# Optimization experiments

Hardware: AMD Instinct MI355X
Metric: run time of the kernel (lower is better)

## Reference

```python
import jax, jax.numpy as jnp
from jax import lax
import numpy as np

# Geometry derived from module.calibrate() for input [2,64,768,768], k=3, s=1, bcount=(16,16)
N, CIN, COUT, H, W = 2, 64, 64, 768, 768
K, STRIDE = 3, 1
BC = 16            # block count per spatial dim
PAD = 1            # total pad 2 -> 1 each side (H and W)
BSIZE = 50         # gathered block size (input space, padded input is 770)
BOUT = 48          # conv output size per block
BSTR = 48          # block stride (= bsize - k + stride); also scatter stride
NBLK = 256
BN_EPS = 1e-3


def setup_inputs() -> dict:
    key = jax.random.key(0)
    ks = jax.random.split(key, 7)
    x = jax.random.normal(ks[0], (N, CIN, H, W), jnp.float32)
    conv_w = jax.random.normal(ks[1], (COUT, CIN, K, K), jnp.float32) * 0.05
    conv_b = jax.random.normal(ks[2], (COUT,), jnp.float32) * 0.1
    gamma = jax.random.uniform(ks[3], (COUT,), jnp.float32, 0.5, 1.5)
    beta = jax.random.normal(ks[4], (COUT,), jnp.float32) * 0.1
    run_mean = jax.random.normal(ks[5], (COUT,), jnp.float32) * 0.1
    run_var = jax.random.uniform(ks[6], (COUT,), jnp.float32, 0.5, 1.5)
    # unique active blocks (n, bh, bw) as in ReduceMask.active_block_indices
    rng = np.random.default_rng(0)
    all_blocks = np.stack(np.meshgrid(np.arange(N), np.arange(BC), np.arange(BC),
                                      indexing='ij'), axis=-1).reshape(-1, 3)
    sel = rng.permutation(all_blocks.shape[0])[:NBLK]
    abi = jnp.asarray(all_blocks[sel], jnp.int32)
    return dict(x=x, conv_w=conv_w, conv_b=conv_b, gamma=gamma, beta=beta,
                run_mean=run_mean, run_var=run_var, active_block_indices=abi)


def reference(x, conv_w, conv_b, gamma, beta, run_mean, run_var, active_block_indices):
    # pad as in F.pad(padding_params)
    xp = jnp.pad(x, ((0, 0), (0, 0), (PAD, PAD), (PAD, PAD)))  # [N,C,770,770]
    nidx = active_block_indices[:, 0]                          # [B]
    hh = active_block_indices[:, 1][:, None] * BSTR + jnp.arange(BSIZE)[None, :]  # [B,50]
    ww = active_block_indices[:, 2][:, None] * BSTR + jnp.arange(BSIZE)[None, :]  # [B,50]
    # sparse_gather: extract [B,50,50,C] blocks (vectorized advanced indexing)
    xp_nhwc = xp.transpose(0, 2, 3, 1)
    p = xp_nhwc[nidx[:, None, None], hh[:, :, None], ww[:, None, :]]   # [B,50,50,C]
    p = p.transpose(0, 3, 1, 2)                                        # [B,C,50,50]
    # conv2d (VALID) + bias
    q = lax.conv_general_dilated(p, conv_w, (STRIDE, STRIDE), 'VALID')
    q = q + conv_b[None, :, None, None]                                # [B,COUT,48,48]
    # BatchNorm (inference: running stats) + ReLU
    inv = gamma / jnp.sqrt(run_var + BN_EPS)
    q = q * inv[None, :, None, None] + (beta - run_mean * inv)[None, :, None, None]
    q = jax.nn.relu(q)
    # sparse_scatter (add=False) into [N,COUT,768,768]; blocks are non-overlapping
    ho = active_block_indices[:, 1][:, None] * BSTR + jnp.arange(BOUT)[None, :]
    wo = active_block_indices[:, 2][:, None] * BSTR + jnp.arange(BOUT)[None, :]
    y = jnp.zeros((N, H, W, COUT), x.dtype)
    y = y.at[nidx[:, None, None], ho[:, :, None], wo[:, None, :]].set(q.transpose(0, 2, 3, 1))
    return y.transpose(0, 3, 1, 2)
```

## Files before the change

kernel.cpp:

```cpp
#include <hip/hip_runtime.h>


typedef __attribute__((ext_vector_type(8))) short short8;
typedef __attribute__((ext_vector_type(4))) float floatx4;

#define WS_SCALE 0
#define WS_SHIFT 64
#define WS_FLAGS 128
#define WS_WA    640

#define CONV_WGS 1536
#define ZERO_WGS 4096

#define LDS_BUF 4864

__device__ __forceinline__ short f2bf(float f) {
  unsigned u = __builtin_bit_cast(unsigned, f);
  u += 0x7fffu + ((u >> 16) & 1u);
  return (short)(u >> 16);
}

__global__ __launch_bounds__(256) void prep_kernel(
    const float* __restrict__ conv_w,
    const float* __restrict__ conv_b,
    const float* __restrict__ gamma,
    const float* __restrict__ beta,
    const float* __restrict__ run_mean,
    const float* __restrict__ run_var,
    const int* __restrict__ abi,
    float* __restrict__ ws) {
  int tid = threadIdx.x;
  if (blockIdx.x == 0) {
    int* flags = (int*)(ws + WS_FLAGS);
    flags[tid] = 0;
    flags[tid + 256] = 0;
    __syncthreads();
    int n = abi[3 * tid + 0];
    int bh = abi[3 * tid + 1];
    int bw = abi[3 * tid + 2];
    flags[n * 256 + bh * 16 + bw] = 1;
    if (tid < 64) {
      float inv = gamma[tid] * rsqrtf(run_var[tid] + 1e-3f);
      ws[WS_SCALE + tid] = inv;
      ws[WS_SHIFT + tid] = (conv_b[tid] - run_mean[tid]) * inv + beta[tid];
    }
  }
  short* wa = (short*)(ws + WS_WA);
  for (int d = blockIdx.x * 256 + tid; d < 49152; d += 64 * 256) {
    int j = d & 7;
    int q = (d >> 3) & 3;
    int cout = (d >> 5) & 63;
    int ks = d >> 11;
    int kt = ks % 3;
    int cc = ks / 3;
    int tap = kt * 4 + q;
    short v = 0;
    if (tap < 9) {
      int ci = cc * 8 + j;
      int dy = tap / 3;
      int dx = tap - dy * 3;
      v = f2bf(conv_w[((cout * 64 + ci) * 3 + dy) * 3 + dx]);
    }
    wa[d] = v;
  }
}

__global__ __launch_bounds__(512, 4) void main_kernel(
    const float* __restrict__ x,
    const float* __restrict__ ws_f,
    const int* __restrict__ abi,
    float* __restrict__ out) {
  __shared__ __align__(16) short lds[3 * LDS_BUF];

  int b = blockIdx.x;
  int tid = threadIdx.x;

  if (b >= CONV_WGS) {
    const int* flags = (const int*)(ws_f + WS_FLAGS);
    int z = b - CONV_WGS;
    int tile = z >> 3;
    int part = z & 7;
    if (flags[tile]) return;
    int n = tile >> 8;
    int bh = (tile >> 4) & 15;
    int bw = tile & 15;
    float* base = out + (((n * 64 + part * 8) * 768 + bh * 48)) * 768 + bw * 48;
    float4 zv = make_float4(0.f, 0.f, 0.f, 0.f);
#pragma unroll
    for (int i = 0; i < 9; ++i) {
      int idx = i * 512 + tid;
      int f = idx % 12;
      int t2 = idx / 12;
      int rr = t2 % 48;
      int c = t2 / 48;
      *((float4*)(base + (c * 768 + rr) * (size_t)768) + f) = zv;
    }
    return;
  }

  int blk = b / 6;
  int strip = b - blk * 6;
  int n = abi[3 * blk + 0];
  int bh = abi[3 * blk + 1];
  int bw = abi[3 * blk + 2];
  int h0 = bh * 48 + strip * 8;
  int w0 = bw * 48;

  int lane = tid & 63;
  int wv = tid >> 6;
  int ln15 = lane & 15;
  int quad = lane >> 4;

  const float* xn = x + (size_t)n * 64 * 768 * 768;
  const short* wa = (const short*)(ws_f + WS_WA);
  const short* wap = wa + ln15 * 32 + quad * 8;

  if (tid < 8) {
#pragma unroll
    for (int bb = 0; bb < 3; ++bb) {
      lds[bb * LDS_BUF + 4560 + tid] = 0;
      lds[bb * LDS_BUF + 4704 + tid] = 0;
      lds[bb * LDS_BUF + 4848 + tid] = 0;
    }
  }

  int bA[3];
#pragma unroll
  for (int kt = 0; kt < 3; ++kt) {
    int tap = kt * 4 + quad;
    if (tap < 9) {
      int dy = tap / 3;
      int dx = tap - dy * 3;
      int cx = ln15 + dx;
      bA[kt] = ((wv + dy) * 57 + cx + (cx >> 3)) * 16;
    } else {
      bA[kt] = 9120;
    }
  }

  auto load_chunk = [&](int cc8, float4* pf) {
#pragma unroll
    for (int i = 0; i < 3; ++i) {
      int e = i * 512 + tid;
      float4 v = make_float4(0.f, 0.f, 0.f, 0.f);
      if (e < 1120) {
        int f = e % 14;
        int t = e / 14;
        int r = t % 10;
        int ci = t / 10;
        int gh = h0 - 1 + r;
        int gw0 = w0 - 4 + 4 * f;
        if ((unsigned)gh < 768u) {
          const float* rp = xn + ((size_t)(cc8 + ci) * 768 + gh) * 768;
          if (gw0 >= 0 && gw0 <= 764) {
            v = *(const float4*)(rp + gw0);
          } else {
#pragma unroll
            for (int j = 0; j < 4; ++j) {
              int gw = gw0 + j;
              if ((unsigned)gw < 768u) ((float*)&v)[j] = rp[gw];
            }
          }
        }
      }
      pf[i] = v;
    }
  };
  auto store_chunk = [&](short* dst, const float4* pf) {
#pragma unroll
    for (int i = 0; i < 3; ++i) {
      int e = i * 512 + tid;
      if (e < 1120) {
        int f = e % 14;
        int t = e / 14;
        int r = t % 10;
        int ci = t / 10;
        const float* vp = (const float*)&pf[i];
#pragma unroll
        for (int j = 0; j < 4; ++j) {
          int c = 4 * f - 3 + j;
          if ((unsigned)c < 50u) {
            int u = r * 57 + c + (c >> 3);
            dst[u * 8 + ci] = f2bf(vp[j]);
          }
        }
      }
    }
  };

  float4 pf[3];
  load_chunk(0, pf);
  store_chunk(lds, pf);
  load_chunk(8, pf);

  floatx4 acc[3][4];
#pragma unroll
  for (int c16 = 0; c16 < 3; ++c16)
#pragma unroll
    for (int mt = 0; mt < 4; ++mt)
      acc[c16][mt] = (floatx4){0.f, 0.f, 0.f, 0.f};

  int rb = 0;
  for (int cc = 0; cc < 8; ++cc) {
    __syncthreads();
    int sb = (rb == 2) ? 0 : rb + 1;
    if (cc < 7) store_chunk(lds + sb * LDS_BUF, pf);
    if (cc < 6) load_chunk((cc + 2) * 8, pf);
    const char* lb = (const char*)(lds + rb * LDS_BUF);
#pragma unroll
    for (int kt = 0; kt < 3; ++kt) {
      int ks = cc * 3 + kt;
      short8 af[4];
#pragma unroll
      for (int mt = 0; mt < 4; ++mt)
        af[mt] = *(const short8*)(wap + ks * 2048 + mt * 512);
#pragma unroll
      for (int c16 = 0; c16 < 3; ++c16) {
        short8 bf = *(const short8*)(lb + bA[kt] + c16 * 288);
#pragma unroll
        for (int mt = 0; mt < 4; ++mt)
          acc[c16][mt] = __builtin_amdgcn_mfma_f32_16x16x32_bf16(
              af[mt], bf, acc[c16][mt], 0, 0, 0);
      }
    }
    rb = sb;
  }

  const float* scale = ws_f + WS_SCALE;
  const float* shift = ws_f + WS_SHIFT;
  float* op = out + (size_t)n * 64 * 768 * 768 + (size_t)(h0 + wv) * 768 + (w0 + ln15);
#pragma unroll
  for (int mt = 0; mt < 4; ++mt) {
#pragma unroll
    for (int reg = 0; reg < 4; ++reg) {
      int cout = mt * 16 + quad * 4 + reg;
      float sc = scale[cout];
      float sh = shift[cout];
#pragma unroll
      for (int c16 = 0; c16 < 3; ++c16) {
        float vv = fmaf(acc[c16][mt][reg], sc, sh);
        vv = vv > 0.f ? vv : 0.f;
        op[(size_t)cout * 589824 + c16 * 16] = vv;
      }
    }
  }
}

extern "C" void kernel_launch(void* const* d_in, const int* in_sizes, int n_in,
                              void* d_out, int out_size, void* d_ws, size_t ws_size,
                              hipStream_t stream) {
  const float* x = (const float*)d_in[0];
  const float* conv_w = (const float*)d_in[1];
  const float* conv_b = (const float*)d_in[2];
  const float* gamma = (const float*)d_in[3];
  const float* beta = (const float*)d_in[4];
  const float* run_mean = (const float*)d_in[5];
  const float* run_var = (const float*)d_in[6];
  const int* abi = (const int*)d_in[7];
  float* out = (float*)d_out;
  float* ws = (float*)d_ws;

  prep_kernel<<<64, 256, 0, stream>>>(conv_w, conv_b, gamma, beta,
                                      run_mean, run_var, abi, ws);
  main_kernel<<<CONV_WGS + ZERO_WGS, 512, 0, stream>>>(x, ws, abi, out);
}
```

Measured before the change: 585.5 us.

## Stage conv weight slices into LDS via async global_load_lds double buffer

Weight fragments were read by every wave straight from global memory. They are now copied per channel-chunk into a double-buffered LDS slice using global_load_lds, and the prep kernel reorders the weights so each lane's fragment is contiguous. The input staging drops from a triple to a double buffer, with one barrier at the end of each iteration. The aim is to cut repeated global and L2 traffic for weights and hide it behind compute. Total LDS per workgroup grows to about 44KB, which may reduce how many workgroups fit per CU. The barrier may also force waits on in-flight prefetch loads.

Result: faster. 558.0 us (-4.7%).

```diff
diff --git a/kernel.cpp b/kernel.cpp
--- a/kernel.cpp
+++ b/kernel.cpp
@@ -13,6 +13,7 @@
 #define ZERO_WGS 4096
 
 #define LDS_BUF 4864
+#define WSLICE  6144
 
 __device__ __forceinline__ short f2bf(float f) {
   unsigned u = __builtin_bit_cast(unsigned, f);
@@ -48,14 +49,18 @@
   short* wa = (short*)(ws + WS_WA);
   for (int d = blockIdx.x * 256 + tid; d < 49152; d += 64 * 256) {
     int j = d & 7;
-    int q = (d >> 3) & 3;
-    int cout = (d >> 5) & 63;
-    int ks = d >> 11;
+    int g = d >> 3;
+    int i4q = g & 63;
+    int ln15 = i4q >> 2;
+    int quad = i4q & 3;
+    int mt = (g >> 6) & 3;
+    int ks = g >> 8;
     int kt = ks % 3;
     int cc = ks / 3;
-    int tap = kt * 4 + q;
+    int tap = kt * 4 + quad;
     short v = 0;
     if (tap < 9) {
+      int cout = mt * 16 + ln15;
       int ci = cc * 8 + j;
       int dy = tap / 3;
       int dx = tap - dy * 3;
@@ -70,7 +75,8 @@
     const float* __restrict__ ws_f,
     const int* __restrict__ abi,
     float* __restrict__ out) {
-  __shared__ __align__(16) short lds[3 * LDS_BUF];
+  __shared__ __align__(16) short lds_i[2][LDS_BUF];
+  __shared__ __align__(16) short lds_w[2][WSLICE];
 
   int b = blockIdx.x;
   int tid = threadIdx.x;
@@ -113,14 +119,14 @@
 
   const float* xn = x + (size_t)n * 64 * 768 * 768;
   const short* wa = (const short*)(ws_f + WS_WA);
-  const short* wap = wa + ln15 * 32 + quad * 8;
+  int wOff = (ln15 * 4 + quad) * 8;
 
   if (tid < 8) {
 #pragma unroll
-    for (int bb = 0; bb < 3; ++bb) {
-      lds[bb * LDS_BUF + 4560 + tid] = 0;
-      lds[bb * LDS_BUF + 4704 + tid] = 0;
-      lds[bb * LDS_BUF + 4848 + tid] = 0;
+    for (int bb = 0; bb < 2; ++bb) {
+      lds_i[bb][4560 + tid] = 0;
+      lds_i[bb][4704 + tid] = 0;
+      lds_i[bb][4848 + tid] = 0;
     }
   }
 
@@ -137,6 +143,18 @@
       bA[kt] = 9120;
     }
   }
+
+  auto wload = [&](int cc, int wsel) {
+    const short* src = wa + (size_t)cc * WSLICE;
+    __builtin_amdgcn_global_load_lds(
+        (const __attribute__((address_space(1))) void*)(src + tid * 8),
+        (__attribute__((address_space(3))) void*)&lds_w[wsel][tid * 8], 16, 0, 0);
+    if (tid < 256)
+      __builtin_amdgcn_global_load_lds(
+          (const __attribute__((address_space(1))) void*)(src + 4096 + tid * 8),
+          (__attribute__((address_space(3))) void*)&lds_w[wsel][4096 + tid * 8],
+          16, 0, 0);
+  };
 
   auto load_chunk = [&](int cc8, float4* pf) {
 #pragma unroll
@@ -189,8 +207,9 @@
   };
 
   float4 pf[3];
+  wload(0, 0);
   load_chunk(0, pf);
-  store_chunk(lds, pf);
+  store_chunk(lds_i[0], pf);
   load_chunk(8, pf);
 
   floatx4 acc[3][4];
@@ -200,20 +219,23 @@
     for (int mt = 0; mt < 4; ++mt)
       acc[c16][mt] = (floatx4){0.f, 0.f, 0.f, 0.f};
 
-  int rb = 0;
+  __syncthreads();
+
   for (int cc = 0; cc < 8; ++cc) {
-    __syncthreads();
-    int sb = (rb == 2) ? 0 : rb + 1;
-    if (cc < 7) store_chunk(lds + sb * LDS_BUF, pf);
+    int bsel = cc & 1;
+    if (cc < 7) {
+      wload(cc + 1, bsel ^ 1);
+      store_chunk(lds_i[bsel ^ 1], pf);
+    }
     if (cc < 6) load_chunk((cc + 2) * 8, pf);
-    const char* lb = (const char*)(lds + rb * LDS_BUF);
+    const char* lb = (const char*)lds_i[bsel];
+    const short* lw = lds_w[bsel];
 #pragma unroll
     for (int kt = 0; kt < 3; ++kt) {
-      int ks = cc * 3 + kt;
       short8 af[4];
 #pragma unroll
       for (int mt = 0; mt < 4; ++mt)
-        af[mt] = *(const short8*)(wap + ks * 2048 + mt * 512);
+        af[mt] = *(const short8*)(lw + wOff + ((kt * 4 + mt) << 9));
 #pragma unroll
       for (int c16 = 0; c16 < 3; ++c16) {
         short8 bf = *(const short8*)(lb + bA[kt] + c16 * 288);
@@ -223,7 +245,7 @@
               af[mt], bf, acc[c16][mt], 0, 0, 0);
       }
     }
-    rb = sb;
+    if (cc < 7) __syncthreads();
   }
 
   const float* scale = ws_f + WS_SCALE;
```
